# Kernel optimization log

Measured on AMD Instinct MI355X. Metric: run time of the kernel, lower is better.

## Reference

```python
import jax, jax.numpy as jnp
import numpy as np

HID = 128   # hidden_dim
NCLS = 10   # n_classes
B = 64      # number of graphs in the batched heterograph
NC, NP, NN = 100000, 400000, 150000  # component / port / net node counts
E = 400000  # edges per edge type


def setup_inputs() -> dict:
    key = jax.random.key(0)
    ks = jax.random.split(key, 32)
    f32 = jnp.float32

    def w(k, shape, fan_in):
        return jax.random.normal(k, shape, dtype=f32) * (1.0 / np.sqrt(fan_in))

    inp = {
        "h_comp": jax.random.normal(ks[0], (NC, 1), f32),
        "h_port": jax.random.normal(ks[1], (NP, 2), f32),
        "h_net": jax.random.normal(ks[2], (NN, 1), f32),
        "e_cp_src": jax.random.randint(ks[3], (E,), 0, NC, dtype=jnp.int32),
        "e_cp_dst": jax.random.randint(ks[4], (E,), 0, NP, dtype=jnp.int32),
        "e_pn_src": jax.random.randint(ks[5], (E,), 0, NP, dtype=jnp.int32),
        "e_pn_dst": jax.random.randint(ks[6], (E,), 0, NN, dtype=jnp.int32),
        "gid_comp": jnp.sort(jax.random.randint(ks[7], (NC,), 0, B, dtype=jnp.int32)),
        "gid_port": jnp.sort(jax.random.randint(ks[8], (NP,), 0, B, dtype=jnp.int32)),
        "gid_net": jnp.sort(jax.random.randint(ks[9], (NN,), 0, B, dtype=jnp.int32)),
        # GraphConv weights/biases per (layer, edge_type)
        "W1_cp": w(ks[10], (1, HID), 1), "b1_cp": jnp.zeros((HID,), f32),
        "W1_pn": w(ks[11], (2, HID), 2), "b1_pn": jnp.zeros((HID,), f32),
        "W2_cp": w(ks[12], (HID, HID), HID), "b2_cp": jnp.zeros((HID,), f32),
        "W2_pn": w(ks[13], (HID, HID), HID), "b2_pn": jnp.zeros((HID,), f32),
        "W3_cp": w(ks[14], (HID, HID), HID), "b3_cp": jnp.zeros((HID,), f32),
        "W3_pn": w(ks[15], (HID, HID), HID), "b3_pn": jnp.zeros((HID,), f32),
        # classify MLP (input dim 4 = 1+2+1 pooled original features)
        "Wc1": w(ks[16], (4, HID), 4), "bc1": jnp.zeros((HID,), f32),
        "Wc2": w(ks[17], (HID, HID), HID), "bc2": jnp.zeros((HID,), f32),
        "Wc3": w(ks[18], (HID, NCLS), HID), "bc3": jnp.zeros((NCLS,), f32),
    }
    return inp


def reference(h_comp, h_port, h_net,
              e_cp_src, e_cp_dst, e_pn_src, e_pn_dst,
              gid_comp, gid_port, gid_net,
              W1_cp, b1_cp, W1_pn, b1_pn,
              W2_cp, b2_cp, W2_pn, b2_pn,
              W3_cp, b3_cp, W3_pn, b3_pn,
              Wc1, bc1, Wc2, bc2, Wc3, bc3):
    seg = jax.ops.segment_sum

    # --- HeteroGraphConv layers (faithful to original forward, including its
    # bug: DGL HeteroGraphConv drops node types with no incoming relation, so
    # 'component' vanishes after conv1 and 'port' after conv2; conv3 runs on an
    # empty dict; conv outputs are never written back to g, hence dead code).
    # GraphConv(norm='none'): dst = sum_{edges} (x_src @ W) + b
    port1 = jax.nn.relu(seg((h_comp @ W1_cp)[e_cp_src], e_cp_dst, num_segments=NP) + b1_cp)
    net1 = jax.nn.relu(seg((h_port @ W1_pn)[e_pn_src], e_pn_dst, num_segments=NN) + b1_pn)
    net2 = jax.nn.relu(seg((port1 @ W2_pn)[e_pn_src], e_pn_dst, num_segments=NN) + b2_pn)
    # conv3: skipped entirely (no src types remain in the feature dict)
    del net1, net2  # never used by the original module's output path

    # --- dgl.mean_nodes reads g.nodes[*].data['h'] = ORIGINAL input features
    def gmean(x, gid):
        s = seg(x, gid, num_segments=B)
        c = seg(jnp.ones((x.shape[0], 1), x.dtype), gid, num_segments=B)
        return s / jnp.maximum(c, 1.0)

    hg = jnp.concatenate([gmean(h_comp, gid_comp),
                          gmean(h_port, gid_port),
                          gmean(h_net, gid_net)], axis=1)  # [B, 4]

    h = jax.nn.relu(hg @ Wc1 + bc1)
    h = jax.nn.relu(h @ Wc2 + bc2)
    return h @ Wc3 + bc3  # [B, n_classes]
```

## Files before the change

### kernel.cpp

```cpp
#include <hip/hip_runtime.h>
#include <hip/hip_bf16.h>


#define NGRAPH 64


#define NB_COMP 128
#define NB_PORT 384
#define NB_NET  128

template <int NF>
__device__ void reduce_type(const float* __restrict__ h, const int* __restrict__ gid, int n,
                            float* __restrict__ gsum, float* __restrict__ gcnt,
                            int nblocks, int bid) {
    __shared__ float bins[NGRAPH][4];
    for (int i = threadIdx.x; i < NGRAPH * 4; i += blockDim.x) ((float*)bins)[i] = 0.f;
    __syncthreads();

    int nv = (n + 3) >> 2;
    int per = (nv + nblocks - 1) / nblocks;
    int start = bid * per;
    int end = min(nv, start + per);

    int cur = -1;
    float s0 = 0.f, s1 = 0.f, cnt = 0.f;

    for (int iv = start + (int)threadIdx.x; iv < end; iv += (int)blockDim.x) {
        int i = iv * 4;
        int g[4];
        float v0[4], v1[4];
        if (i + 3 < n) {
            int4 g4 = ((const int4*)gid)[iv];
            g[0] = g4.x; g[1] = g4.y; g[2] = g4.z; g[3] = g4.w;
            if (NF == 1) {
                float4 hv = ((const float4*)h)[iv];
                v0[0] = hv.x; v0[1] = hv.y; v0[2] = hv.z; v0[3] = hv.w;
            } else {
                float4 ha = ((const float4*)h)[iv * 2];
                float4 hb = ((const float4*)h)[iv * 2 + 1];
                v0[0] = ha.x; v1[0] = ha.y; v0[1] = ha.z; v1[1] = ha.w;
                v0[2] = hb.x; v1[2] = hb.y; v0[3] = hb.z; v1[3] = hb.w;
            }
        } else {
#pragma unroll
            for (int t = 0; t < 4; ++t) {
                if (i + t < n) {
                    g[t] = gid[i + t];
                    if (NF == 1) { v0[t] = h[i + t]; }
                    else { v0[t] = h[(i + t) * 2]; v1[t] = h[(i + t) * 2 + 1]; }
                } else {
                    g[t] = -2;
                    v0[t] = 0.f; v1[t] = 0.f;
                }
            }
        }
#pragma unroll
        for (int t = 0; t < 4; ++t) {
            if (g[t] == -2) continue;
            if (g[t] != cur) {
                if (cur >= 0) {
                    atomicAdd(&bins[cur][0], s0);
                    if (NF == 2) atomicAdd(&bins[cur][1], s1);
                    atomicAdd(&bins[cur][2], cnt);
                }
                cur = g[t]; s0 = 0.f; s1 = 0.f; cnt = 0.f;
            }
            s0 += v0[t];
            if (NF == 2) s1 += v1[t];
            cnt += 1.f;
        }
    }
    if (cur >= 0) {
        atomicAdd(&bins[cur][0], s0);
        if (NF == 2) atomicAdd(&bins[cur][1], s1);
        atomicAdd(&bins[cur][2], cnt);
    }
    __syncthreads();

    for (int g = threadIdx.x; g < NGRAPH; g += blockDim.x) {
        float c = bins[g][2];
        if (c != 0.f) {
            if (NF == 1) {
                atomicAdd(&gsum[g], bins[g][0]);
            } else {
                atomicAdd(&gsum[g * 2 + 0], bins[g][0]);
                atomicAdd(&gsum[g * 2 + 1], bins[g][1]);
            }
            atomicAdd(&gcnt[g], c);
        }
    }
}

__global__ __launch_bounds__(256) void reduce_kernel(
    const float* __restrict__ h_comp, const float* __restrict__ h_port,
    const float* __restrict__ h_net,
    const int* __restrict__ gid_comp, const int* __restrict__ gid_port,
    const int* __restrict__ gid_net,
    int n_comp, int n_port, int n_net,
    float* __restrict__ ws) {
    int bid = blockIdx.x;
    if (bid < NB_COMP) {
        reduce_type<1>(h_comp, gid_comp, n_comp, ws + 0, ws + 64, NB_COMP, bid);
    } else if (bid < NB_COMP + NB_PORT) {
        reduce_type<2>(h_port, gid_port, n_port, ws + 128, ws + 256, NB_PORT, bid - NB_COMP);
    } else {
        reduce_type<1>(h_net, gid_net, n_net, ws + 320, ws + 384, NB_NET, bid - NB_COMP - NB_PORT);
    }
}

__global__ __launch_bounds__(128) void mlp_kernel(
    const float* __restrict__ ws,
    const float* __restrict__ Wc1, const float* __restrict__ bc1,
    const float* __restrict__ Wc2, const float* __restrict__ bc2,
    const float* __restrict__ Wc3, const float* __restrict__ bc3,
    float* __restrict__ out) {
    __shared__ float h1[128];
    __shared__ float h2[128];

    int b = blockIdx.x;
    int j = threadIdx.x;

    float cc = fmaxf(ws[64 + b], 1.f);
    float g0 = ws[b] / cc;
    float cp = fmaxf(ws[256 + b], 1.f);
    float g1 = ws[128 + 2 * b] / cp;
    float g2 = ws[128 + 2 * b + 1] / cp;
    float cn = fmaxf(ws[384 + b], 1.f);
    float g3 = ws[320 + b] / cn;

    float v = g0 * Wc1[j] + g1 * Wc1[128 + j] + g2 * Wc1[256 + j] + g3 * Wc1[384 + j] + bc1[j];
    h1[j] = fmaxf(v, 0.f);
    __syncthreads();

    float acc = bc2[j];
#pragma unroll 8
    for (int k = 0; k < 128; k += 4) {
        float4 hh = *(const float4*)&h1[k];
        float w0 = Wc2[(k + 0) * 128 + j];
        float w1 = Wc2[(k + 1) * 128 + j];
        float w2 = Wc2[(k + 2) * 128 + j];
        float w3 = Wc2[(k + 3) * 128 + j];
        acc += hh.x * w0 + hh.y * w1 + hh.z * w2 + hh.w * w3;
    }
    h2[j] = fmaxf(acc, 0.f);
    __syncthreads();

    if (j < 10) {
        float a = bc3[j];
#pragma unroll 8
        for (int k = 0; k < 128; ++k) a += h2[k] * Wc3[k * 10 + j];
        out[b * 10 + j] = a;
    }
}

extern "C" void kernel_launch(void* const* d_in, const int* in_sizes, int n_in,
                              void* d_out, int out_size, void* d_ws, size_t ws_size,
                              hipStream_t stream) {
    const float* h_comp = (const float*)d_in[0];
    const float* h_port = (const float*)d_in[1];
    const float* h_net  = (const float*)d_in[2];
    const int* gid_comp = (const int*)d_in[7];
    const int* gid_port = (const int*)d_in[8];
    const int* gid_net  = (const int*)d_in[9];
    const float* Wc1 = (const float*)d_in[22];
    const float* bc1 = (const float*)d_in[23];
    const float* Wc2 = (const float*)d_in[24];
    const float* bc2 = (const float*)d_in[25];
    const float* Wc3 = (const float*)d_in[26];
    const float* bc3 = (const float*)d_in[27];

    int n_comp = in_sizes[0];
    int n_port = in_sizes[1] / 2;
    int n_net  = in_sizes[2];

    float* ws = (float*)d_ws;
    float* out = (float*)d_out;

    hipMemsetAsync(ws, 0, 448 * sizeof(float), stream);

    reduce_kernel<<<NB_COMP + NB_PORT + NB_NET, 256, 0, stream>>>(
        h_comp, h_port, h_net, gid_comp, gid_port, gid_net,
        n_comp, n_port, n_net, ws);

    mlp_kernel<<<NGRAPH, 128, 0, stream>>>(ws, Wc1, bc1, Wc2, bc2, Wc3, bc3, out);
}
```

Measured before the change: 122.9 us.

## Fuse reduction and MLP into one kernel with ticket-based grid handoff

Merges the per-graph mean reduction and the classifier MLP into a single kernel. The first 64 blocks to finish the reduction spin on a global counter until all blocks are done, then each computes one graph's MLP, which removes a kernel launch. The grid shrinks from 640 to 256 blocks so all blocks can be co-resident and the spin-wait cannot deadlock. Shared-memory bins are replicated four ways to cut atomic contention, and the MLP layers are split across more threads. The risks are spin-wait overhead and less parallelism for the memory-bound reduction.

After: 129.1 us. 1.05x slower.

```diff
diff --git a/kernel.cpp b/kernel.cpp
--- a/kernel.cpp
+++ b/kernel.cpp
@@ -3,24 +3,26 @@
 
 
 #define NGRAPH 64
-
-
-#define NB_COMP 128
-#define NB_PORT 384
-#define NB_NET  128
+#define NB_COMP 40
+#define NB_PORT 172
+#define NB_NET  44
+#define GRID (NB_COMP + NB_PORT + NB_NET)
+
+
+__device__ __forceinline__ float ws_read(float* p) {
+    return atomicAdd(p, 0.0f);
+}
 
 template <int NF>
 __device__ void reduce_type(const float* __restrict__ h, const int* __restrict__ gid, int n,
                             float* __restrict__ gsum, float* __restrict__ gcnt,
+                            float (*bins)[NGRAPH][4],
                             int nblocks, int bid) {
-    __shared__ float bins[NGRAPH][4];
-    for (int i = threadIdx.x; i < NGRAPH * 4; i += blockDim.x) ((float*)bins)[i] = 0.f;
-    __syncthreads();
-
     int nv = (n + 3) >> 2;
     int per = (nv + nblocks - 1) / nblocks;
     int start = bid * per;
     int end = min(nv, start + per);
+    int set = threadIdx.x & 3;
 
     int cur = -1;
     float s0 = 0.f, s1 = 0.f, cnt = 0.f;
@@ -59,9 +61,9 @@
             if (g[t] == -2) continue;
             if (g[t] != cur) {
                 if (cur >= 0) {
-                    atomicAdd(&bins[cur][0], s0);
-                    if (NF == 2) atomicAdd(&bins[cur][1], s1);
-                    atomicAdd(&bins[cur][2], cnt);
+                    atomicAdd(&bins[set][cur][0], s0);
+                    if (NF == 2) atomicAdd(&bins[set][cur][1], s1);
+                    atomicAdd(&bins[set][cur][2], cnt);
                 }
                 cur = g[t]; s0 = 0.f; s1 = 0.f; cnt = 0.f;
             }
@@ -71,85 +73,121 @@
         }
     }
     if (cur >= 0) {
-        atomicAdd(&bins[cur][0], s0);
-        if (NF == 2) atomicAdd(&bins[cur][1], s1);
-        atomicAdd(&bins[cur][2], cnt);
+        atomicAdd(&bins[set][cur][0], s0);
+        if (NF == 2) atomicAdd(&bins[set][cur][1], s1);
+        atomicAdd(&bins[set][cur][2], cnt);
     }
     __syncthreads();
 
     for (int g = threadIdx.x; g < NGRAPH; g += blockDim.x) {
-        float c = bins[g][2];
+        float c = bins[0][g][2] + bins[1][g][2] + bins[2][g][2] + bins[3][g][2];
         if (c != 0.f) {
+            float a0 = bins[0][g][0] + bins[1][g][0] + bins[2][g][0] + bins[3][g][0];
             if (NF == 1) {
-                atomicAdd(&gsum[g], bins[g][0]);
+                atomicAdd(&gsum[g], a0);
             } else {
-                atomicAdd(&gsum[g * 2 + 0], bins[g][0]);
-                atomicAdd(&gsum[g * 2 + 1], bins[g][1]);
+                float a1 = bins[0][g][1] + bins[1][g][1] + bins[2][g][1] + bins[3][g][1];
+                atomicAdd(&gsum[g * 2 + 0], a0);
+                atomicAdd(&gsum[g * 2 + 1], a1);
             }
             atomicAdd(&gcnt[g], c);
         }
     }
 }
 
-__global__ __launch_bounds__(256) void reduce_kernel(
+__global__ __launch_bounds__(256) void fused_kernel(
     const float* __restrict__ h_comp, const float* __restrict__ h_port,
     const float* __restrict__ h_net,
     const int* __restrict__ gid_comp, const int* __restrict__ gid_port,
     const int* __restrict__ gid_net,
     int n_comp, int n_port, int n_net,
-    float* __restrict__ ws) {
-    int bid = blockIdx.x;
-    if (bid < NB_COMP) {
-        reduce_type<1>(h_comp, gid_comp, n_comp, ws + 0, ws + 64, NB_COMP, bid);
-    } else if (bid < NB_COMP + NB_PORT) {
-        reduce_type<2>(h_port, gid_port, n_port, ws + 128, ws + 256, NB_PORT, bid - NB_COMP);
-    } else {
-        reduce_type<1>(h_net, gid_net, n_net, ws + 320, ws + 384, NB_NET, bid - NB_COMP - NB_PORT);
-    }
-}
-
-__global__ __launch_bounds__(128) void mlp_kernel(
-    const float* __restrict__ ws,
     const float* __restrict__ Wc1, const float* __restrict__ bc1,
     const float* __restrict__ Wc2, const float* __restrict__ bc2,
     const float* __restrict__ Wc3, const float* __restrict__ bc3,
-    float* __restrict__ out) {
+    float* __restrict__ ws, float* __restrict__ out) {
+    __shared__ float bins[4][NGRAPH][4];
+    __shared__ int ticket;
+    __shared__ float hgs[4];
     __shared__ float h1[128];
+    __shared__ float part[2][128];
     __shared__ float h2[128];
-
-    int b = blockIdx.x;
-    int j = threadIdx.x;
-
-    float cc = fmaxf(ws[64 + b], 1.f);
-    float g0 = ws[b] / cc;
-    float cp = fmaxf(ws[256 + b], 1.f);
-    float g1 = ws[128 + 2 * b] / cp;
-    float g2 = ws[128 + 2 * b + 1] / cp;
-    float cn = fmaxf(ws[384 + b], 1.f);
-    float g3 = ws[320 + b] / cn;
-
-    float v = g0 * Wc1[j] + g1 * Wc1[128 + j] + g2 * Wc1[256 + j] + g3 * Wc1[384 + j] + bc1[j];
-    h1[j] = fmaxf(v, 0.f);
-    __syncthreads();
-
-    float acc = bc2[j];
-#pragma unroll 8
-    for (int k = 0; k < 128; k += 4) {
-        float4 hh = *(const float4*)&h1[k];
-        float w0 = Wc2[(k + 0) * 128 + j];
-        float w1 = Wc2[(k + 1) * 128 + j];
-        float w2 = Wc2[(k + 2) * 128 + j];
-        float w3 = Wc2[(k + 3) * 128 + j];
-        acc += hh.x * w0 + hh.y * w1 + hh.z * w2 + hh.w * w3;
-    }
-    h2[j] = fmaxf(acc, 0.f);
-    __syncthreads();
-
-    if (j < 10) {
-        float a = bc3[j];
-#pragma unroll 8
-        for (int k = 0; k < 128; ++k) a += h2[k] * Wc3[k * 10 + j];
-        out[b * 10 + j] = a;
+    __shared__ float l3[16][12];
+
+    int tid = threadIdx.x;
+    int bid = blockIdx.x;
+    int* counter = (int*)(ws + 448);
+
+    for (int i = tid; i < 4 * NGRAPH * 4; i += blockDim.x) ((float*)bins)[i] = 0.f;
+    __syncthreads();
+
+    if (bid < NB_COMP) {
+        reduce_type<1>(h_comp, gid_comp, n_comp, ws + 0, ws + 64, bins, NB_COMP, bid);
+    } else if (bid < NB_COMP + NB_PORT) {
+        reduce_type<2>(h_port, gid_port, n_port, ws + 128, ws + 256, bins, NB_PORT, bid - NB_COMP);
+    } else {
+        reduce_type<1>(h_net, gid_net, n_net, ws + 320, ws + 384, bins, NB_NET, bid - NB_COMP - NB_PORT);
+    }
+    __syncthreads();
+
+    if (tid == 0) {
+        __threadfence();
+        ticket = atomicAdd(counter, 1);
+    }
+    __syncthreads();
+    int my = ticket;
+    if (my >= NGRAPH) return;
+
+    int g = my;
+    if (tid == 0) {
+        while (atomicAdd(counter, 0) < GRID) __builtin_amdgcn_s_sleep(2);
+        float cc = fmaxf(ws_read(ws + 64 + g), 1.f);
+        float cp = fmaxf(ws_read(ws + 256 + g), 1.f);
+        float cn = fmaxf(ws_read(ws + 384 + g), 1.f);
+        hgs[0] = ws_read(ws + g) / cc;
+        hgs[1] = ws_read(ws + 128 + 2 * g) / cp;
+        hgs[2] = ws_read(ws + 128 + 2 * g + 1) / cp;
+        hgs[3] = ws_read(ws + 320 + g) / cn;
+    }
+    __syncthreads();
+
+    if (tid < 128) {
+        float v = hgs[0] * Wc1[tid] + hgs[1] * Wc1[128 + tid] +
+                  hgs[2] * Wc1[256 + tid] + hgs[3] * Wc1[384 + tid] + bc1[tid];
+        h1[tid] = fmaxf(v, 0.f);
+    }
+    __syncthreads();
+
+    {
+        int j = tid & 127;
+        int h = tid >> 7;
+        float acc = 0.f;
+#pragma unroll
+        for (int kk = 0; kk < 64; kk += 4) {
+            int k = h * 64 + kk;
+            float4 hh = *(const float4*)&h1[k];
+            acc += hh.x * Wc2[(k + 0) * 128 + j] + hh.y * Wc2[(k + 1) * 128 + j] +
+                   hh.z * Wc2[(k + 2) * 128 + j] + hh.w * Wc2[(k + 3) * 128 + j];
+        }
+        part[h][j] = acc;
+    }
+    __syncthreads();
+    if (tid < 128) h2[tid] = fmaxf(part[0][tid] + part[1][tid] + bc2[tid], 0.f);
+    __syncthreads();
+
+    if (tid < 160) {
+        int c = tid % 10;
+        int seg = tid / 10;
+        float a = 0.f;
+#pragma unroll
+        for (int k = seg * 8; k < seg * 8 + 8; ++k) a += h2[k] * Wc3[k * 10 + c];
+        l3[seg][c] = a;
+    }
+    __syncthreads();
+    if (tid < 10) {
+        float a = bc3[tid];
+#pragma unroll
+        for (int s = 0; s < 16; ++s) a += l3[s][tid];
+        out[g * 10 + tid] = a;
     }
 }
 
@@ -176,11 +214,10 @@
     float* ws = (float*)d_ws;
     float* out = (float*)d_out;
 
-    hipMemsetAsync(ws, 0, 448 * sizeof(float), stream);
-
-    reduce_kernel<<<NB_COMP + NB_PORT + NB_NET, 256, 0, stream>>>(
+    hipMemsetAsync(ws, 0, 452 * sizeof(float), stream);
+
+    fused_kernel<<<GRID, 256, 0, stream>>>(
         h_comp, h_port, h_net, gid_comp, gid_port, gid_net,
-        n_comp, n_port, n_net, ws);
-
-    mlp_kernel<<<NGRAPH, 128, 0, stream>>>(ws, Wc1, bc1, Wc2, bc2, Wc3, bc3, out);
-}
+        n_comp, n_port, n_net,
+        Wc1, bc1, Wc2, bc2, Wc3, bc3, ws, out);
+}
```
